# Kernel optimization log

Measured on AMD Instinct MI355X. Metric: run time of the kernel, lower is better.

The kernel has to match this reference:

```python
import jax, jax.numpy as jnp
import numpy as np

K, S, P = 3, 2, 2  # kernel_size, stride, padding (dilation=1)


def _unfold(xp, k, s, oh, ow):
    """Extract k*k strided patches from a padded array.

    xp: (..., Hp, Wp) -> (..., k*k, oh, ow), window-position ordering (kh, kw)
    matching torch.nn.Unfold (channel-major handled by caller).
    """
    return jnp.stack(
        [xp[..., i:i + s * (oh - 1) + 1:s, j:j + s * (ow - 1) + 1:s]
         for i in range(K) for j in range(K)],
        axis=-3,
    )


def setup_inputs() -> dict:
    key = jax.random.key(0)
    x = jax.random.normal(key, (8, 256, 128, 128), dtype=jnp.float32)
    return {"x": x}


def reference(x):
    b, c, h, w = x.shape
    oh = (h - K + 2 * P) // S + 1
    ow = (w - K + 2 * P) // S + 1

    # channel-wise L2 norm, computed BEFORE unfolding (padding contributes 0 either way)
    n = jnp.sqrt(jnp.sum(x * x, axis=1))            # (b, h, w)
    n_pad = jnp.pad(n, ((0, 0), (P, P), (P, P)))
    n_patch = _unfold(n_pad, K, S, oh, ow)          # (b, k*k, oh, ow)
    # weighting_fn = softmax over the k*k window positions (torch dim=1 of unfolded norm)
    wts = jax.nn.softmax(n_patch, axis=1)           # (b, k*k, oh, ow)

    x_pad = jnp.pad(x, ((0, 0), (0, 0), (P, P), (P, P)))
    x_patch = _unfold(x_pad, K, S, oh, ow)          # (b, c, k*k, oh, ow)

    # weighted sum over window positions
    return jnp.sum(wts[:, None] * x_patch, axis=2)  # (b, c, oh, ow)
```

## Files before the change

### kernel.cpp

```cpp
#include <hip/hip_runtime.h>
#include <math.h>

#define BATCH 8
#define CH    256
#define H     128
#define W     128
#define HW    (H * W)
#define OH    65
#define OW    65
#define NPIX  (OH * OW)

__global__ __launch_bounds__(256) void norm_kernel(const float4* __restrict__ x4,
                                                   float* __restrict__ nrm) {
    const int b    = blockIdx.x >> 6;
    const int t    = blockIdx.x & 63;
    const int lane = threadIdx.x & 63;
    const int wv   = threadIdx.x >> 6;

    const float4* p = x4 + (size_t)(b * CH + wv * 64) * (HW / 4) + t * 64 + lane;
    float4 a = {0.f, 0.f, 0.f, 0.f};
    #pragma unroll 8
    for (int c = 0; c < 64; ++c) {
        float4 v = p[(size_t)c * (HW / 4)];
        a.x += v.x * v.x; a.y += v.y * v.y;
        a.z += v.z * v.z; a.w += v.w * v.w;
    }
    __shared__ float part[4][256];
    ((float4*)part[wv])[lane] = a;
    __syncthreads();
    float s = part[0][threadIdx.x] + part[1][threadIdx.x]
            + part[2][threadIdx.x] + part[3][threadIdx.x];
    nrm[(size_t)b * HW + t * 256 + threadIdx.x] = sqrtf(s);
}

__global__ __launch_bounds__(256) void pool_kernel(const float* __restrict__ x,
                                                   const float* __restrict__ nrm,
                                                   float* __restrict__ out) {
    const int b    = blockIdx.x & 7;
    const int g    = blockIdx.x >> 3;
    const int lane = threadIdx.x & 63;
    const int wv   = threadIdx.x >> 6;
    const int c    = g * 4 + wv;

    const float2* xr = (const float2*)(x + (size_t)(b * CH + c) * HW);
    const float2* nr = (const float2*)(nrm + (size_t)b * HW);
    float*        op = out + (size_t)(b * CH + c) * NPIX;

    float2 xv2 = xr[lane], nv2 = nr[lane];
    float2 xv0 = xv2, xv1 = xv2;
    float2 nv0 = nv2, nv1 = nv2;

    #pragma unroll 4
    for (int oh = 0; oh < OH; ++oh) {
        if (oh > 0) {
            xv0 = xv2; nv0 = nv2;
            const int r1 = 2 * oh - 1;
            const int r2 = (2 * oh < H) ? 2 * oh : H - 1;
            xv1 = xr[r1 * 64 + lane]; nv1 = nr[r1 * 64 + lane];
            xv2 = xr[r2 * 64 + lane]; nv2 = nr[r2 * 64 + lane];
        }
        const bool rv0 = (oh > 0);
        const bool rv2 = (oh < OH - 1);
        const bool cOK = (lane < 63);

        float nd0 = __shfl_down(nv0.x, 1);
        float nd1 = __shfl_down(nv1.x, 1);
        float nd2 = __shfl_down(nv2.x, 1);

        float n00 = rv0 ? nv0.x : 0.f, n01 = rv0 ? nv0.y : 0.f;
        float n02 = (rv0 && cOK) ? nd0 : 0.f;
        float n10 = rv0 ? nv1.x : 0.f, n11 = rv0 ? nv1.y : 0.f;
        float n12 = (rv0 && cOK) ? nd1 : 0.f;
        float n20 = rv2 ? nv2.x : 0.f, n21 = rv2 ? nv2.y : 0.f;
        float n22 = (rv2 && cOK) ? nd2 : 0.f;

        float m = 0.f;
        m = fmaxf(m, n00); m = fmaxf(m, n01); m = fmaxf(m, n02);
        m = fmaxf(m, n10); m = fmaxf(m, n11); m = fmaxf(m, n12);
        m = fmaxf(m, n20); m = fmaxf(m, n21); m = fmaxf(m, n22);

        float e00 = __expf(n00 - m), e01 = __expf(n01 - m), e02 = __expf(n02 - m);
        float e10 = __expf(n10 - m), e11 = __expf(n11 - m), e12 = __expf(n12 - m);
        float e20 = __expf(n20 - m), e21 = __expf(n21 - m), e22 = __expf(n22 - m);
        float denom = e00 + e01 + e02 + e10 + e11 + e12 + e20 + e21 + e22;
        float inv = 1.0f / denom;

        float w00 = rv0 ? e00 * inv : 0.f, w01 = rv0 ? e01 * inv : 0.f;
        float w02 = (rv0 && cOK) ? e02 * inv : 0.f;
        float w10 = rv0 ? e10 * inv : 0.f, w11 = rv0 ? e11 * inv : 0.f;
        float w12 = (rv0 && cOK) ? e12 * inv : 0.f;
        float w20 = rv2 ? e20 * inv : 0.f, w21 = rv2 ? e21 * inv : 0.f;
        float w22 = (rv2 && cOK) ? e22 * inv : 0.f;

        float xd0 = __shfl_down(xv0.x, 1);
        float xd1 = __shfl_down(xv1.x, 1);
        float xd2 = __shfl_down(xv2.x, 1);

        float o = w00 * xv0.x + w01 * xv0.y + w02 * xd0
                + w10 * xv1.x + w11 * xv1.y + w12 * xd1
                + w20 * xv2.x + w21 * xv2.y + w22 * xd2;
        op[oh * OW + 1 + lane] = o;

        if (lane == 0) {
            float m0 = fmaxf(fmaxf(0.f, n00), fmaxf(n10, n20));
            float q0 = __expf(n00 - m0);
            float q1 = __expf(n10 - m0);
            float q2 = __expf(n20 - m0);
            float d0 = 6.f * __expf(0.f - m0) + q0 + q1 + q2;
            float i0 = 1.0f / d0;
            float t0 = rv0 ? q0 * i0 : 0.f;
            float t1 = rv0 ? q1 * i0 : 0.f;
            float t2 = rv2 ? q2 * i0 : 0.f;
            op[oh * OW] = t0 * xv0.x + t1 * xv1.x + t2 * xv2.x;
        }
    }
}

extern "C" void kernel_launch(void* const* d_in, const int* in_sizes, int n_in,
                              void* d_out, int out_size, void* d_ws, size_t ws_size,
                              hipStream_t stream) {
    const float* x = (const float*)d_in[0];
    float* out  = (float*)d_out;
    float* nbuf = (float*)d_ws;

    norm_kernel<<<512, 256, 0, stream>>>((const float4*)x, nbuf);
    pool_kernel<<<512, 256, 0, stream>>>(x, nbuf, out);
}
```

Before: 236.3 us.

## Process four channels per wave and split output rows across blocks

```diff
diff --git a/kernel.cpp b/kernel.cpp
--- a/kernel.cpp
+++ b/kernel.cpp
@@ -33,45 +33,77 @@
     nrm[(size_t)b * HW + t * 256 + threadIdx.x] = sqrtf(s);
 }
 
+#define NQ 8
 __global__ __launch_bounds__(256) void pool_kernel(const float* __restrict__ x,
                                                    const float* __restrict__ nrm,
                                                    float* __restrict__ out) {
     const int b    = blockIdx.x & 7;
-    const int g    = blockIdx.x >> 3;
+    const int r    = blockIdx.x >> 3;
+    const int g2   = r >> 3;
+    const int q    = r & 7;
     const int lane = threadIdx.x & 63;
     const int wv   = threadIdx.x >> 6;
-    const int c    = g * 4 + wv;
+    const int c0   = g2 * 16 + wv * 4;
+    const int oh0  = q * 8;
+    const int ohN  = (q == NQ - 1) ? 9 : 8;
 
-    const float2* xr = (const float2*)(x + (size_t)(b * CH + c) * HW);
+    const float2* xp = (const float2*)(x + (size_t)(b * CH + c0) * HW);
     const float2* nr = (const float2*)(nrm + (size_t)b * HW);
-    float*        op = out + (size_t)(b * CH + c) * NPIX;
+    float*       op0 = out + (size_t)(b * CH + c0) * NPIX;
 
-    float2 xv2 = xr[lane], nv2 = nr[lane];
-    float2 xv0 = xv2, xv1 = xv2;
-    float2 nv0 = nv2, nv1 = nv2;
+    float2 a0[4], a1[4], a2[4];
+    float2 n0, n1, n2;
 
-    #pragma unroll 4
-    for (int oh = 0; oh < OH; ++oh) {
-        if (oh > 0) {
-            xv0 = xv2; nv0 = nv2;
-            const int r1 = 2 * oh - 1;
-            const int r2 = (2 * oh < H) ? 2 * oh : H - 1;
-            xv1 = xr[r1 * 64 + lane]; nv1 = nr[r1 * 64 + lane];
-            xv2 = xr[r2 * 64 + lane]; nv2 = nr[r2 * 64 + lane];
+    if (oh0 == 0) {
+        n2 = nr[lane];  n0 = n2;  n1 = n2;
+        #pragma unroll
+        for (int cc = 0; cc < 4; ++cc) {
+            a2[cc] = xp[(size_t)cc * (HW / 2) + lane];
+            a0[cc] = a2[cc];  a1[cc] = a2[cc];
+        }
+    } else {
+        const int r0i = 2 * oh0 - 2, r1i = 2 * oh0 - 1, r2i = 2 * oh0;
+        n0 = nr[r0i * 64 + lane];
+        n1 = nr[r1i * 64 + lane];
+        n2 = nr[r2i * 64 + lane];
+        #pragma unroll
+        for (int cc = 0; cc < 4; ++cc) {
+            const size_t cb = (size_t)cc * (HW / 2);
+            a0[cc] = xp[cb + r0i * 64 + lane];
+            a1[cc] = xp[cb + r1i * 64 + lane];
+            a2[cc] = xp[cb + r2i * 64 + lane];
+        }
+    }
+
+    for (int i = 0; i < ohN; ++i) {
+        const int oh = oh0 + i;
+        if (i > 0) {
+            const int r1i = 2 * oh - 1;
+            const int r2i = (2 * oh < H) ? 2 * oh : H - 1;
+            n0 = n2;
+            n1 = nr[r1i * 64 + lane];
+            n2 = nr[r2i * 64 + lane];
+            #pragma unroll
+            for (int cc = 0; cc < 4; ++cc) {
+                const size_t cb = (size_t)cc * (HW / 2);
+                a0[cc] = a2[cc];
+                a1[cc] = xp[cb + r1i * 64 + lane];
+                a2[cc] = xp[cb + r2i * 64 + lane];
+            }
         }
         const bool rv0 = (oh > 0);
         const bool rv2 = (oh < OH - 1);
         const bool cOK = (lane < 63);
 
-        float nd0 = __shfl_down(nv0.x, 1);
-        float nd1 = __shfl_down(nv1.x, 1);
-        float nd2 = __shfl_down(nv2.x, 1);
+        float nd0 = __shfl_down(n0.x, 1);
+        float nd1 = __shfl_down(n1.x, 1);
+        float nd2 = __shfl_down(n2.x, 1);
 
-        float n00 = rv0 ? nv0.x : 0.f, n01 = rv0 ? nv0.y : 0.f;
+        float n00 = rv0 ? n0.x : 0.f, n01 = rv0 ? n0.y : 0.f;
         float n02 = (rv0 && cOK) ? nd0 : 0.f;
-        float n10 = rv0 ? nv1.x : 0.f, n11 = rv0 ? nv1.y : 0.f;
+        float n10 = rv0 ? n1.x : 0.f, n11 = rv0 ? n1.y : 0.f;
         float n12 = (rv0 && cOK) ? nd1 : 0.f;
-        float n20 = rv2 ? nv2.x : 0.f, n21 = rv2 ? nv2.y : 0.f;
+        float n20 = rv2 ? n2.x : 0.f, n21 = rv2 ? n2.y : 0.f;
         float n22 = (rv2 && cOK) ? nd2 : 0.f;
 
         float m = 0.f;
@@ -92,26 +124,28 @@
         float w20 = rv2 ? e20 * inv : 0.f, w21 = rv2 ? e21 * inv : 0.f;
         float w22 = (rv2 && cOK) ? e22 * inv : 0.f;
 
-        float xd0 = __shfl_down(xv0.x, 1);
-        float xd1 = __shfl_down(xv1.x, 1);
-        float xd2 = __shfl_down(xv2.x, 1);
+        float m0 = fmaxf(fmaxf(0.f, n00), fmaxf(n10, n20));
+        float p0 = __expf(n00 - m0);
+        float p1 = __expf(n10 - m0);
+        float p2 = __expf(n20 - m0);
+        float d0 = 6.f * __expf(0.f - m0) + p0 + p1 + p2;
+        float i0 = 1.0f / d0;
+        float t0 = rv0 ? p0 * i0 : 0.f;
+        float t1 = rv0 ? p1 * i0 : 0.f;
+        float t2 = rv2 ? p2 * i0 : 0.f;
 
-        float o = w00 * xv0.x + w01 * xv0.y + w02 * xd0
-                + w10 * xv1.x + w11 * xv1.y + w12 * xd1
-                + w20 * xv2.x + w21 * xv2.y + w22 * xd2;
-        op[oh * OW + 1 + lane] = o;
-
-        if (lane == 0) {
-            float m0 = fmaxf(fmaxf(0.f, n00), fmaxf(n10, n20));
-            float q0 = __expf(n00 - m0);
-            float q1 = __expf(n10 - m0);
-            float q2 = __expf(n20 - m0);
-            float d0 = 6.f * __expf(0.f - m0) + q0 + q1 + q2;
-            float i0 = 1.0f / d0;
-            float t0 = rv0 ? q0 * i0 : 0.f;
-            float t1 = rv0 ? q1 * i0 : 0.f;
-            float t2 = rv2 ? q2 * i0 : 0.f;
-            op[oh * OW] = t0 * xv0.x + t1 * xv1.x + t2 * xv2.x;
+        #pragma unroll
+        for (int cc = 0; cc < 4; ++cc) {
+            float xd0 = __shfl_down(a0[cc].x, 1);
+            float xd1 = __shfl_down(a1[cc].x, 1);
+            float xd2 = __shfl_down(a2[cc].x, 1);
+            float o = w00 * a0[cc].x + w01 * a0[cc].y + w02 * xd0
+                    + w10 * a1[cc].x + w11 * a1[cc].y + w12 * xd1
+                    + w20 * a2[cc].x + w21 * a2[cc].y + w22 * xd2;
+            float* op = op0 + (size_t)cc * NPIX;
+            op[oh * OW + 1 + lane] = o;
+            if (lane == 0)
+                op[oh * OW] = t0 * a0[cc].x + t1 * a1[cc].x + t2 * a2[cc].x;
         }
     }
 }
@@ -124,5 +158,5 @@
     float* nbuf = (float*)d_ws;
 
     norm_kernel<<<512, 256, 0, stream>>>((const float4*)x, nbuf);
-    pool_kernel<<<512, 256, 0, stream>>>(x, nbuf, out);
+    pool_kernel<<<1024, 256, 0, stream>>>(x, nbuf, out);
 }
```

Result: faster. 224.1 us (-5.1%).
